# Kernel optimization log

Measured on AMD Instinct MI355X. Metric: run time of the kernel, lower is better.

Reference implementation:

```python
import jax, jax.numpy as jnp
import numpy as np
import math

B, N, D, H, K, W = 2, 2048, 512, 8, 64, 5
HD = D // H      # head_dim = 64
QC = HD // 4     # per-head quaternion component = 16
QI = D // 4      # full-model quaternion component = 128


def _qlinear(x, r, i, j, k, b):
    # Hamilton-product weight matrix, as built in QLinear.forward
    Wm = jnp.concatenate([
        jnp.concatenate([r, -i, -j, -k], 1),
        jnp.concatenate([i,  r, -k,  j], 1),
        jnp.concatenate([j,  k,  r, -i], 1),
        jnp.concatenate([k, -j,  i,  r], 1)], 0)
    return x @ Wm.T + b


def _layernorm(x, g, b, eps=1e-5):
    m = x.mean(-1, keepdims=True)
    v = ((x - m) ** 2).mean(-1, keepdims=True)
    return (x - m) / jnp.sqrt(v + eps) * g + b


def _forward(query, key, value, cross_context, density_feat, mask, time_idx,
             q_r, q_i, q_j, q_k, q_b, k_r, k_i, k_j, k_k, k_b,
             v_w, v_b, o_w, o_b, thr, dm1_w, dm1_b, dm2_w, dm2_b,
             ef, ec, ev_w, ev_b, ln_g, ln_b):
    spike_slope = 5.0
    # ---- QuaternionSpikeAttention (cross_ctx=True, dropout inactive in eval) ----
    q = _qlinear(query, q_r, q_i, q_j, q_k, q_b)
    k = _qlinear(key, k_r, k_i, k_j, k_k, k_b) + _qlinear(cross_context, k_r, k_i, k_j, k_k, k_b)
    v = jnp.concatenate([value, cross_context], -1) @ v_w.T + v_b
    qh = q.reshape(B, N, H, HD)
    kh = k.reshape(B, N, H, HD)
    vh = v.reshape(B, N, H, HD)
    # sum of the 4 quaternion-component dot products == full dot over head_dim
    scores = jnp.einsum('bmhd,bnhd->bhmn', qh, kh) / math.sqrt(QC)
    scores = jnp.clip(scores, -6.0, 6.0)
    base_thr = jax.nn.softplus(thr)
    hdm = jax.nn.gelu(density_feat @ dm1_w.T + dm1_b, approximate=False)
    d_shift = (hdm @ dm2_w.T + dm2_b)[..., 0]                # [B, N]
    threshold = base_thr + d_shift[:, None, None, :] * 0.1   # varies over key index
    gate = jax.nn.sigmoid(spike_slope * (scores - threshold))
    mod = scores * (1.0 + 2.0 * gate)
    m2 = mask[:, None, :, None] * mask[:, None, None, :]     # [B,1,M,N] outer mask
    mod = jnp.where(m2 == 0, -10000.0, mod)
    wts = jax.nn.softmax(jnp.clip(mod, -30.0, 30.0), axis=-1)
    attn = jnp.einsum('bhmn,bnhd->bmhd', wts, vh).reshape(B, N, D)
    attn = attn @ o_w.T + o_b
    # ---- TemporalEventConvolution ----
    order = jnp.argsort(time_idx, axis=1)
    qs = jnp.take_along_axis(query, order[..., None], axis=1)
    ms = jnp.take_along_axis(mask, order, axis=1)
    half = W // 2
    qp = jnp.pad(qs, ((0, 0), (half, half), (0, 0)))
    qwin = jnp.stack([qp[:, w:w + N] for w in range(W)], axis=2)  # [B,N,W,D]
    # quaternion-split filter matching collapses to a full dot over D
    act = jnp.einsum('bnwd,kwd->bnk', qwin, ef) / math.sqrt(QI)
    act = jnp.where(ms[..., None] == 0, -10000.0, act)
    act = jax.nn.softmax(act, axis=-1)
    ctx = act @ ec                                            # [B,N,D]
    ctx = _layernorm(ctx @ ev_w.T + ev_b, ln_g, ln_b) * ms[..., None]
    inv = jnp.argsort(order, axis=1)
    ctx = jnp.take_along_axis(ctx, inv[..., None], axis=1) * mask[..., None]
    return attn + ctx


def setup_inputs() -> dict:
    key0 = jax.random.key(0)
    ks = jax.random.split(key0, 24)
    lim = math.sqrt(6.0 / (QI + QI))
    def xav(k):
        return jax.random.uniform(k, (QI, QI), jnp.float32, -lim, lim)
    def lin(k, o, i):
        l = math.sqrt(1.0 / i)
        return jax.random.uniform(k, (o, i), jnp.float32, -l, l)
    return {
        'query': jax.random.normal(ks[0], (B, N, D), jnp.float32),
        'key': jax.random.normal(ks[1], (B, N, D), jnp.float32),
        'value': jax.random.normal(ks[2], (B, N, D), jnp.float32),
        'cross_context': jax.random.normal(ks[3], (B, N, D), jnp.float32),
        'density_feat': jax.random.normal(ks[4], (B, N, 3), jnp.float32),
        'mask': jnp.ones((B, N), jnp.float32),
        'time_idx': jax.random.randint(ks[5], (B, N), 0, 1000000),
        'q_r': xav(ks[6]), 'q_i': xav(ks[7]), 'q_j': xav(ks[8]), 'q_k': xav(ks[9]),
        'q_b': jnp.zeros((D,), jnp.float32),
        'k_r': xav(ks[10]), 'k_i': xav(ks[11]), 'k_j': xav(ks[12]), 'k_k': xav(ks[13]),
        'k_b': jnp.zeros((D,), jnp.float32),
        'v_w': lin(ks[14], D, 2 * D), 'v_b': jnp.zeros((D,), jnp.float32),
        'o_w': lin(ks[15], D, D), 'o_b': jnp.zeros((D,), jnp.float32),
        'thr': jnp.float32(-1.0),
        'dm1_w': lin(ks[16], 16, 3), 'dm1_b': jnp.zeros((16,), jnp.float32),
        'dm2_w': jnp.zeros((1, 16), jnp.float32), 'dm2_b': jnp.zeros((1,), jnp.float32),
        'ef': jax.random.normal(ks[17], (K, W, D), jnp.float32) * 0.02,
        'ec': jax.random.normal(ks[18], (K, D), jnp.float32) * 0.02,
        'ev_w': lin(ks[19], D, D), 'ev_b': jnp.zeros((D,), jnp.float32),
        'ln_g': jnp.ones((D,), jnp.float32), 'ln_b': jnp.zeros((D,), jnp.float32),
    }


def reference(query, key, value, cross_context, density_feat, mask, time_idx,
              q_r, q_i, q_j, q_k, q_b, k_r, k_i, k_j, k_k, k_b,
              v_w, v_b, o_w, o_b, thr, dm1_w, dm1_b, dm2_w, dm2_b,
              ef, ec, ev_w, ev_b, ln_g, ln_b):
    return _forward(query, key, value, cross_context, density_feat, mask, time_idx,
                    q_r, q_i, q_j, q_k, q_b, k_r, k_i, k_j, k_k, k_b,
                    v_w, v_b, o_w, o_b, thr, dm1_w, dm1_b, dm2_w, dm2_b,
                    ef, ec, ev_w, ev_b, ln_g, ln_b)
```

## Files before the change

kernel.cpp:

```cpp
#include <hip/hip_runtime.h>
#include <math.h>

#define BB 2
#define NN 2048
#define DDIM 512
#define HH 8
#define HDIM 64
#define BN 4096

#define WS_WMQ   0
#define WS_WMK   262144
#define WS_THRK  524288
#define WS_ORDER 528384
#define WS_DKW   532480
#define WS_W5    1843200
#define WS_Q     2105344
#define WS_K     4202496
#define WS_V     6299648
#define PLANE_US 2097152

typedef short bf16x8 __attribute__((ext_vector_type(8)));
typedef float f32x4  __attribute__((ext_vector_type(4)));

__device__ __forceinline__ float4 ld4(const float* p) { return *(const float4*)p; }

__device__ __forceinline__ float red16_max(float v) {
  v = fmaxf(v, __shfl_xor(v, 1, 64));
  v = fmaxf(v, __shfl_xor(v, 2, 64));
  v = fmaxf(v, __shfl_xor(v, 4, 64));
  v = fmaxf(v, __shfl_xor(v, 8, 64));
  return v;
}
__device__ __forceinline__ float red16_sum(float v) {
  v += __shfl_xor(v, 1, 64);
  v += __shfl_xor(v, 2, 64);
  v += __shfl_xor(v, 4, 64);
  v += __shfl_xor(v, 8, 64);
  return v;
}

__device__ __forceinline__ unsigned short f2bu(float f) {
  unsigned u = __float_as_uint(f);
  unsigned r = 0x7FFFu + ((u >> 16) & 1u);
  return (unsigned short)((u + r) >> 16);
}
__device__ __forceinline__ float bu2f(unsigned short u) {
  return __uint_as_float(((unsigned)u) << 16);
}
__device__ __forceinline__ void split2(float x, unsigned short& hi, unsigned short& lo) {
  hi = f2bu(x);
  lo = f2bu(x - bu2f(hi));
}

__global__ __launch_bounds__(256) void build_wm_kernel(
    const float* __restrict__ qr, const float* __restrict__ qi,
    const float* __restrict__ qj, const float* __restrict__ qk,
    const float* __restrict__ kr, const float* __restrict__ ki,
    const float* __restrict__ kj, const float* __restrict__ kk,
    unsigned short* __restrict__ wmqH, unsigned short* __restrict__ wmqL,
    unsigned short* __restrict__ wmkH, unsigned short* __restrict__ wmkL)
{
  int idx = blockIdx.x * 256 + threadIdx.x;
  int sel = idx >> 18;
  int r   = idx & 262143;
  int p = r >> 9, q = r & 511;
  int pb = p >> 7, qb = q >> 7, pr = p & 127, qc = q & 127;
  const int   comp_t[4][4] = {{0,1,2,3},{1,0,3,2},{2,3,0,1},{3,2,1,0}};
  const float sign_t[4][4] = {{1.f,-1.f,-1.f,-1.f},{1.f,1.f,-1.f,1.f},
                              {1.f,1.f,1.f,-1.f},{1.f,-1.f,1.f,1.f}};
  const float* cq[4] = {qr,qi,qj,qk};
  const float* ck[4] = {kr,ki,kj,kk};
  int c = comp_t[pb][qb];
  float s = sign_t[pb][qb];
  const float* src = sel ? ck[c] : cq[c];
  float v = s * src[pr*128 + qc];
  unsigned short hi, lo;
  split2(v, hi, lo);
  if (sel) { wmkH[r] = hi; wmkL[r] = lo; }
  else     { wmqH[r] = hi; wmqL[r] = lo; }
}

__global__ __launch_bounds__(256) void presplit_kernel(
    const float* __restrict__ src, int n4,
    unsigned short* __restrict__ hp, unsigned short* __restrict__ lp)
{
  int i = blockIdx.x * 256 + threadIdx.x;
  if (i >= n4) return;
  float4 v = ((const float4*)src)[i];
  ushort4 h, l;
  split2(v.x, h.x, l.x);  split2(v.y, h.y, l.y);
  split2(v.z, h.z, l.z);  split2(v.w, h.w, l.w);
  ((ushort4*)hp)[i] = h;
  ((ushort4*)lp)[i] = l;
}

__global__ __launch_bounds__(256) void rank_kernel(const int* __restrict__ tidx,
                                                   int* __restrict__ order)
{
  __shared__ int ts[NN];
  int b = blockIdx.y;
  for (int i = threadIdx.x; i < NN; i += 256) ts[i] = tidx[b*NN + i];
  __syncthreads();
  int i = blockIdx.x * 256 + threadIdx.x;
  int ti = ts[i];
  int rank = 0;
  #pragma unroll 4
  for (int j = 0; j < NN; j++) {
    int tj = ts[j];
    rank += (tj < ti || (tj == ti && j < i)) ? 1 : 0;
  }
  order[b*NN + rank] = i;
}

__global__ __launch_bounds__(256) void thr_kernel(
    const float* __restrict__ df, const float* __restrict__ dm1w,
    const float* __restrict__ dm1b, const float* __restrict__ dm2w,
    const float* __restrict__ dm2b, const float* __restrict__ thrp,
    int dm1b_bstride, float* __restrict__ thrK)
{
  int i = blockIdx.x * 256 + threadIdx.x;
  if (i >= BN) return;
  int b = i >> 11;
  const float* bb = dm1b + b*dm1b_bstride;
  float x0 = df[i*3+0], x1 = df[i*3+1], x2 = df[i*3+2];
  float acc = dm2b[0];
  #pragma unroll
  for (int j = 0; j < 16; j++) {
    float h = dm1w[j*3+0]*x0 + dm1w[j*3+1]*x1 + dm1w[j*3+2]*x2 + bb[j];
    h = 0.5f * h * (1.f + erff(h * 0.70710678118654752f));
    acc += h * dm2w[j];
  }
  float tv = thrp[0];
  float base = fmaxf(tv, 0.f) + log1pf(expf(-fabsf(tv)));
  thrK[i] = base + 0.1f * acc;
}

#define GSTR 72
template<int MODE, int OUT, int AP, int BP>
__global__ __launch_bounds__(256) void mgemm_kernel(
    const float* __restrict__ A0, const float* __restrict__ A1,
    const unsigned short* __restrict__ APh, const unsigned short* __restrict__ APl,
    const float* __restrict__ W,
    const unsigned short* __restrict__ BPh, const unsigned short* __restrict__ BPl,
    const float* __restrict__ bias,
    float bias_scale, float scale, float* __restrict__ out,
    int Ka, int N, int ldout)
{
  __shared__ __align__(16) unsigned short AHi[64*GSTR], ALo[64*GSTR];
  __shared__ __align__(16) unsigned short BHi[64*GSTR], BLo[64*GSTR];
  const int t = threadIdx.x;
  const int w = t >> 6, lane = t & 63;
  const int quad = lane >> 4, lm = lane & 15;
  const int m0 = blockIdx.x * 64, n0 = blockIdx.y * 64;
  const int lrr = t >> 4, ld = (t & 15) * 4;

  f32x4 acc[4];
  #pragma unroll
  for (int s = 0; s < 4; s++) acc[s] = (f32x4){0.f,0.f,0.f,0.f};

  for (int k0 = 0; k0 < Ka; k0 += 64) {
    __syncthreads();
    if (AP) {
      #pragma unroll
      for (int i = 0; i < 2; i++) {
        int c = t*2 + i;
        int row = c >> 3, c8 = (c & 7) * 8;
        int off = (m0 + row)*Ka + k0 + c8;
        *(uint4*)&AHi[row*GSTR + c8] = *(const uint4*)&APh[off];
        *(uint4*)&ALo[row*GSTR + c8] = *(const uint4*)&APl[off];
      }
    } else {
      #pragma unroll
      for (int p = 0; p < 4; p++) {
        int row = lrr + p*16;
        float4 av;
        if (MODE == 0) {
          av = ld4(&A0[(size_t)(m0+row)*Ka + k0 + ld]);
        } else if (MODE == 1) {
          float4 x = ld4(&A0[(m0+row)*512 + k0 + ld]);
          float4 y = ld4(&A1[(m0+row)*512 + k0 + ld]);
          av = make_float4(x.x+y.x, x.y+y.y, x.z+y.z, x.w+y.w);
        } else {
          int kg = k0 + ld;
          av = (kg < 512) ? ld4(&A0[(m0+row)*512 + kg])
                          : ld4(&A1[(m0+row)*512 + kg - 512]);
        }
        ushort4 hi, lo;
        split2(av.x, hi.x, lo.x);  split2(av.y, hi.y, lo.y);
        split2(av.z, hi.z, lo.z);  split2(av.w, hi.w, lo.w);
        *(ushort4*)&AHi[row*GSTR + ld] = hi;
        *(ushort4*)&ALo[row*GSTR + ld] = lo;
      }
    }
    if (BP) {
      #pragma unroll
      for (int i = 0; i < 2; i++) {
        int c = t*2 + i;
        int row = c >> 3, c8 = (c & 7) * 8;
        int brow = n0 + row;  if (brow > N-1) brow = N-1;
        int off = brow*Ka + k0 + c8;
        *(uint4*)&BHi[row*GSTR + c8] = *(const uint4*)&BPh[off];
        *(uint4*)&BLo[row*GSTR + c8] = *(const uint4*)&BPl[off];
      }
    } else {
      #pragma unroll
      for (int p = 0; p < 4; p++) {
        int row = lrr + p*16;
        int brow = n0 + row;  if (brow > N-1) brow = N-1;
        float4 wv = ld4(&W[(size_t)brow*Ka + k0 + ld]);
        ushort4 hi, lo;
        split2(wv.x, hi.x, lo.x);  split2(wv.y, hi.y, lo.y);
        split2(wv.z, hi.z, lo.z);  split2(wv.w, hi.w, lo.w);
        *(ushort4*)&BHi[row*GSTR + ld] = hi;
        *(ushort4*)&BLo[row*GSTR + ld] = lo;
      }
    }
    __syncthreads();
    #pragma unroll
    for (int ks = 0; ks < 2; ks++) {
      int arow = (w*16 + lm)*GSTR + ks*32 + quad*8;
      bf16x8 ah = *(const bf16x8*)&AHi[arow];
      bf16x8 al = *(const bf16x8*)&ALo[arow];
      #pragma unroll
      for (int sub = 0; sub < 4; sub++) {
        int baddr = (sub*16 + lm)*GSTR + ks*32 + quad*8;
        bf16x8 bh = *(const bf16x8*)&BHi[baddr];
        bf16x8 bl = *(const bf16x8*)&BLo[baddr];
        acc[sub] = __builtin_amdgcn_mfma_f32_16x16x32_bf16(ah, bh, acc[sub], 0, 0, 0);
        acc[sub] = __builtin_amdgcn_mfma_f32_16x16x32_bf16(ah, bl, acc[sub], 0, 0, 0);
        acc[sub] = __builtin_amdgcn_mfma_f32_16x16x32_bf16(al, bh, acc[sub], 0, 0, 0);
      }
    }
  }
  #pragma unroll
  for (int sub = 0; sub < 4; sub++) {
    int col = n0 + sub*16 + lm;
    if (col >= N) continue;
    float bv = bias ? bias[col] * bias_scale : 0.f;
    if (OUT == 0) {
      #pragma unroll
      for (int r = 0; r < 4; r++) {
        int row = m0 + w*16 + quad*4 + r;
        out[(size_t)row*ldout + col] = acc[sub][r]*scale + bv;
      }
    } else if (OUT == 1) {
      unsigned short* hp = (unsigned short*)out;
      unsigned short* lp = hp + (size_t)4096*ldout;
      #pragma unroll
      for (int r = 0; r < 4; r++) {
        int row = m0 + w*16 + quad*4 + r;
        unsigned short hv, lv;
        split2(acc[sub][r]*scale + bv, hv, lv);
        hp[(size_t)row*ldout + col] = hv;
        lp[(size_t)row*ldout + col] = lv;
      }
    } else {
      unsigned short* hp = (unsigned short*)out;
      unsigned short* lp = hp + (size_t)PLANE_US;
      int hcol = col >> 6, d = col & 63;
      int row0 = m0 + w*16 + quad*4;
      int bb2 = row0 >> 11, n = row0 & 2047;
      unsigned short h0,h1,h2,h3,l0,l1,l2,l3;
      split2(acc[sub][0]*scale + bv, h0, l0);
      split2(acc[sub][1]*scale + bv, h1, l1);
      split2(acc[sub][2]*scale + bv, h2, l2);
      split2(acc[sub][3]*scale + bv, h3, l3);
      size_t vidx = (((size_t)bb2*8 + hcol)*64 + d)*2048 + n;
      *(ushort4*)&hp[vidx] = make_ushort4(h0,h1,h2,h3);
      *(ushort4*)&lp[vidx] = make_ushort4(l0,l1,l2,l3);
    }
  }
}

__global__ __launch_bounds__(256) void t1a_kernel(const float* __restrict__ dkw,
    const int* __restrict__ order, int K, int W, float* __restrict__ w5raw)
{
  int idx = blockIdx.x * 256 + threadIdx.x;
  if (idx >= BN*K) return;
  int k  = idx % K;
  int bn = idx / K;
  int b = bn >> 11, r = bn & 2047;
  const int* ob = order + b*NN;
  int KW = K*W, half = W >> 1;
  float acc = 0.f;
  for (int w = 0; w < W; w++) {
    int rr = r + w - half;
    if (rr < 0 || rr >= NN) continue;
    acc += dkw[(size_t)(b*NN + ob[rr])*KW + k*W + w];
  }
  w5raw[(size_t)(b*NN + ob[r])*K + k] = acc;
}

__global__ __launch_bounds__(256) void t1b_kernel(const float* __restrict__ mask,
    int K, float* __restrict__ w5)
{
  int i = blockIdx.x * 256 + threadIdx.x;
  if (i >= BN) return;
  float* row = w5 + (size_t)i*K;
  if (mask[i] == 0.f) {
    float u = 1.f / (float)K;
    for (int k = 0; k < K; k++) row[k] = u;
    return;
  }
  float mx = -1e30f;
  for (int k = 0; k < K; k++) mx = fmaxf(mx, row[k]);
  float ss = 0.f;
  for (int k = 0; k < K; k++) { float e = __expf(row[k]-mx); row[k] = e; ss += e; }
  float inv = 1.f/ss;
  for (int k = 0; k < K; k++) row[k] *= inv;
}

__global__ __launch_bounds__(256) void ecv_kernel(const float* __restrict__ ec,
    const float* __restrict__ evw, int K, float* __restrict__ ecv)
{
  int idx = blockIdx.x * 256 + threadIdx.x;
  if (idx >= K*512) return;
  int k = idx >> 9, j = idx & 511;
  const float4* e4 = (const float4*)(ec + k*512);
  const float4* w4 = (const float4*)(evw + j*512);
  float acc = 0.f;
  for (int d = 0; d < 128; d++) {
    float4 a = e4[d], b = w4[d];
    acc += a.x*b.x + a.y*b.y + a.z*b.z + a.w*b.w;
  }
  ecv[k*512 + j] = acc;
}

__global__ __launch_bounds__(256) void t2p_kernel(const float* __restrict__ w5,
    const float* __restrict__ ecv, const float* __restrict__ evb,
    int K, float* __restrict__ ctx2)
{
  int idx = blockIdx.x * 256 + threadIdx.x;
  int bn = idx >> 7;
  int q4 = idx & 127;
  const float* wp = w5 + (size_t)bn*K;
  const float4* e4 = (const float4*)ecv;
  float4 bv = ((const float4*)evb)[q4];
  float4 acc = bv;
  for (int k = 0; k < K; k++) {
    float w = wp[k];
    float4 e = e4[k*128 + q4];
    acc.x += w*e.x; acc.y += w*e.y; acc.z += w*e.z; acc.w += w*e.w;
  }
  ((float4*)ctx2)[idx] = acc;
}

#define QSTR 72
__global__ __launch_bounds__(256) void attn_kernel(
    const unsigned short* __restrict__ QHi, const unsigned short* __restrict__ QLo,
    const unsigned short* __restrict__ KHp, const unsigned short* __restrict__ KLp,
    const unsigned short* __restrict__ VtHi, const unsigned short* __restrict__ VtLo,
    const float* __restrict__ thrK, const float* __restrict__ mask,
    unsigned short* __restrict__ AoutH, unsigned short* __restrict__ AoutL)
{
  __shared__ __align__(16) unsigned short KHs[64*QSTR];
  __shared__ __align__(16) unsigned short KLs[64*QSTR];
  __shared__ __align__(16) unsigned short VHs[64*QSTR];
  __shared__ __align__(16) unsigned short VLs[64*QSTR];
  __shared__ float thr_s[64], mk_s[64], mm_s[64];

  const int t = threadIdx.x;
  const int w = t >> 6, lane = t & 63;
  const int quad = lane >> 4, lm = lane & 15;
  const int m0 = blockIdx.x * 64;
  const int bh = blockIdx.y;
  const int b = bh >> 3, h = bh & 7;
  const int base = b*NN*DDIM + h*HDIM;
  const int sr = t >> 3;
  const int sc = (t & 7) * 8;

  bf16x8 qh[2], ql[2];
  {
    size_t qoff = (size_t)(b*NN + m0 + w*16 + lm)*DDIM + h*HDIM + quad*8;
    qh[0] = *(const bf16x8*)&QHi[qoff];
    qh[1] = *(const bf16x8*)&QHi[qoff + 32];
    ql[0] = *(const bf16x8*)&QLo[qoff];
    ql[1] = *(const bf16x8*)&QLo[qoff + 32];
  }
  if (t < 64) mm_s[t] = mask[b*NN + m0 + t];

  f32x4 o_acc[4];
  #pragma unroll
  for (int s = 0; s < 4; s++) o_acc[s] = (f32x4){0.f,0.f,0.f,0.f};
  float m_i[4] = {-1e30f,-1e30f,-1e30f,-1e30f};
  float l_i[4] = {0.f,0.f,0.f,0.f};

  for (int n0 = 0; n0 < NN; n0 += 64) {
    __syncthreads();
    #pragma unroll
    for (int p = 0; p < 2; p++) {
      int row = sr + p*32;
      size_t g  = (size_t)(b*NN + n0 + row)*DDIM + h*HDIM + sc;
      *(uint4*)&KHs[row*QSTR + sc] = *(const uint4*)&KHp[g];
      *(uint4*)&KLs[row*QSTR + sc] = *(const uint4*)&KLp[g];
      size_t gv = ((size_t)bh*HDIM + row)*NN + n0 + sc;
      *(uint4*)&VHs[row*QSTR + sc] = *(const uint4*)&VtHi[gv];
      *(uint4*)&VLs[row*QSTR + sc] = *(const uint4*)&VtLo[gv];
    }
    if (t < 64) { thr_s[t] = thrK[b*NN + n0 + t]; mk_s[t] = mask[b*NN + n0 + t]; }
    __syncthreads();

    f32x4 s_acc[4];
    #pragma unroll
    for (int s = 0; s < 4; s++) s_acc[s] = (f32x4){0.f,0.f,0.f,0.f};
    #pragma unroll
    for (int ks = 0; ks < 2; ks++) {
      #pragma unroll
      for (int sub = 0; sub < 4; sub++) {
        int baddr = (sub*16 + lm)*QSTR + ks*32 + quad*8;
        bf16x8 bh8 = *(const bf16x8*)&KHs[baddr];
        bf16x8 bl8 = *(const bf16x8*)&KLs[baddr];
        s_acc[sub] = __builtin_amdgcn_mfma_f32_16x16x32_bf16(qh[ks], bh8, s_acc[sub], 0, 0, 0);
        s_acc[sub] = __builtin_amdgcn_mfma_f32_16x16x32_bf16(qh[ks], bl8, s_acc[sub], 0, 0, 0);
        s_acc[sub] = __builtin_amdgcn_mfma_f32_16x16x32_bf16(ql[ks], bh8, s_acc[sub], 0, 0, 0);
      }
    }
    __syncthreads();

    float thc5[4], mkc[4];
    #pragma unroll
    for (int sub = 0; sub < 4; sub++) {
      thc5[sub] = 5.f * thr_s[sub*16 + lm];
      mkc[sub] = mk_s[sub*16 + lm];
    }
    float p_[4][4];
    #pragma unroll
    for (int r = 0; r < 4; r++) {
      float mm = mm_s[w*16 + quad*4 + r];
      float rmax = -1e30f;
      float modv[4];
      #pragma unroll
      for (int sub = 0; sub < 4; sub++) {
        float sc2 = s_acc[sub][r]*0.25f;
        sc2 = fminf(fmaxf(sc2,-6.f),6.f);
        float e = __expf(__builtin_fmaf(-5.f, sc2, thc5[sub]));
        float gte = __builtin_amdgcn_rcpf(1.f + e);
        float mv = sc2*(1.f + 2.f*gte);
        if (mm*mkc[sub] == 0.f) mv = -1e4f;
        mv = fminf(fmaxf(mv,-30.f),30.f);
        modv[sub] = mv;
        rmax = fmaxf(rmax, mv);
      }
      rmax = red16_max(rmax);
      float mnew = fmaxf(m_i[r], rmax);
      float scale = __expf(m_i[r]-mnew);
      m_i[r] = mnew;
      float rs = 0.f;
      #pragma unroll
      for (int sub = 0; sub < 4; sub++) { float e = __expf(modv[sub]-mnew); p_[r][sub] = e; rs += e; }
      rs = red16_sum(rs);
      l_i[r] = l_i[r]*scale + rs;
      #pragma unroll
      for (int sub = 0; sub < 4; sub++) o_acc[sub][r] *= scale;
    }
    #pragma unroll
    for (int r = 0; r < 4; r++) {
      int prow = (w*16 + quad*4 + r)*QSTR + lm;
      #pragma unroll
      for (int sub = 0; sub < 4; sub++) {
        unsigned short hi, lo;
        split2(p_[r][sub], hi, lo);
        KHs[prow + sub*16] = hi;
        KLs[prow + sub*16] = lo;
      }
    }
    __syncthreads();

    bf16x8 ph[2], pl[2];
    {
      int arow = (w*16 + lm)*QSTR + quad*8;
      ph[0] = *(const bf16x8*)&KHs[arow];
      ph[1] = *(const bf16x8*)&KHs[arow + 32];
      pl[0] = *(const bf16x8*)&KLs[arow];
      pl[1] = *(const bf16x8*)&KLs[arow + 32];
    }
    #pragma unroll
    for (int ks = 0; ks < 2; ks++) {
      #pragma unroll
      for (int sub = 0; sub < 4; sub++) {
        int baddr = (sub*16 + lm)*QSTR + ks*32 + quad*8;
        bf16x8 vh8 = *(const bf16x8*)&VHs[baddr];
        bf16x8 vl8 = *(const bf16x8*)&VLs[baddr];
        o_acc[sub] = __builtin_amdgcn_mfma_f32_16x16x32_bf16(ph[ks], vh8, o_acc[sub], 0, 0, 0);
        o_acc[sub] = __builtin_amdgcn_mfma_f32_16x16x32_bf16(ph[ks], vl8, o_acc[sub], 0, 0, 0);
        o_acc[sub] = __builtin_amdgcn_mfma_f32_16x16x32_bf16(pl[ks], vh8, o_acc[sub], 0, 0, 0);
      }
    }
  }
  float inv[4];
  #pragma unroll
  for (int r = 0; r < 4; r++) inv[r] = 1.f / l_i[r];
  #pragma unroll
  for (int sub = 0; sub < 4; sub++) {
    #pragma unroll
    for (int r = 0; r < 4; r++) {
      int row = m0 + w*16 + quad*4 + r;
      float val = o_acc[sub][r] * inv[r];
      unsigned short hv, lv;
      split2(val, hv, lv);
      size_t o = (size_t)base + (size_t)row*DDIM + sub*16 + lm;
      AoutH[o] = hv;
      AoutL[o] = lv;
    }
  }
}

__global__ __launch_bounds__(256) void t3_kernel(const float* __restrict__ ctx2,
    const float* __restrict__ lng, const float* __restrict__ lnb,
    const float* __restrict__ mask, const float* __restrict__ outf,
    float* __restrict__ out)
{
  int wid = threadIdx.x >> 6, lane = threadIdx.x & 63;
  int row = blockIdx.x * 4 + wid;
  const float4* x4 = (const float4*)(ctx2 + row*DDIM);
  float4 v0 = x4[lane], v1 = x4[lane+64];
  float s = v0.x+v0.y+v0.z+v0.w + v1.x+v1.y+v1.z+v1.w;
  #pragma unroll
  for (int m = 1; m < 64; m <<= 1) s += __shfl_xor(s, m, 64);
  float mean = s * (1.f/512.f);
  float d0 = v0.x-mean, d1 = v0.y-mean, d2 = v0.z-mean, d3 = v0.w-mean;
  float d4 = v1.x-mean, d5 = v1.y-mean, d6 = v1.z-mean, d7 = v1.w-mean;
  float sq = d0*d0+d1*d1+d2*d2+d3*d3+d4*d4+d5*d5+d6*d6+d7*d7;
  #pragma unroll
  for (int m = 1; m < 64; m <<= 1) sq += __shfl_xor(sq, m, 64);
  float rstd = rsqrtf(sq * (1.f/512.f) + 1e-5f);
  float mk = mask[row];
  float f = mk*mk;
  const float4* g4 = (const float4*)lng;
  const float4* b4 = (const float4*)lnb;
  float4 G0 = g4[lane], G1 = g4[lane+64], B0 = b4[lane], B1 = b4[lane+64];
  float4 O0 = *(const float4*)&outf[row*DDIM + lane*4];
  float4 O1 = *(const float4*)&outf[row*DDIM + (lane+64)*4];
  float4 R0, R1;
  R0.x = O0.x + (d0*rstd*G0.x + B0.x)*f;
  R0.y = O0.y + (d1*rstd*G0.y + B0.y)*f;
  R0.z = O0.z + (d2*rstd*G0.z + B0.z)*f;
  R0.w = O0.w + (d3*rstd*G0.w + B0.w)*f;
  R1.x = O1.x + (d4*rstd*G1.x + B1.x)*f;
  R1.y = O1.y + (d5*rstd*G1.y + B1.y)*f;
  R1.z = O1.z + (d6*rstd*G1.z + B1.z)*f;
  R1.w = O1.w + (d7*rstd*G1.w + B1.w)*f;
  *(float4*)&out[row*DDIM + lane*4] = R0;
  *(float4*)&out[row*DDIM + (lane+64)*4] = R1;
}

__global__ void telem_write_kernel(float val, float* __restrict__ out)
{
  if (threadIdx.x == 0 && blockIdx.x == 0) out[0] = val;
}

extern "C" void kernel_launch(void* const* d_in, const int* in_sizes, int n_in,
                              void* d_out, int out_size, void* d_ws, size_t ws_size,
                              hipStream_t stream)
{
  (void)n_in; (void)out_size; (void)ws_size;
  const float* query = (const float*)d_in[0];
  const float* key_  = (const float*)d_in[1];
  const float* value = (const float*)d_in[2];
  const float* cross = (const float*)d_in[3];
  const float* df    = (const float*)d_in[4];
  const float* mask  = (const float*)d_in[5];
  const int*   tidx  = (const int*)  d_in[6];
  const float* q_r = (const float*)d_in[7],  *q_i = (const float*)d_in[8];
  const float* q_j = (const float*)d_in[9],  *q_k = (const float*)d_in[10];
  const float* q_b = (const float*)d_in[11];
  const float* k_r = (const float*)d_in[12], *k_i = (const float*)d_in[13];
  const float* k_j = (const float*)d_in[14], *k_k = (const float*)d_in[15];
  const float* k_b = (const float*)d_in[16];
  const float* v_w = (const float*)d_in[17], *v_b = (const float*)d_in[18];
  const float* o_w = (const float*)d_in[19], *o_b = (const float*)d_in[20];
  const float* thrp = (const float*)d_in[21];
  const float* dm1w = (const float*)d_in[22], *dm1b = (const float*)d_in[23];
  const float* dm2w = (const float*)d_in[24], *dm2b = (const float*)d_in[25];
  const float* ef   = (const float*)d_in[26], *ec   = (const float*)d_in[27];
  const float* ev_w = (const float*)d_in[28], *ev_b = (const float*)d_in[29];
  const float* lng  = (const float*)d_in[30], *lnb  = (const float*)d_in[31];

  const int s23 = in_sizes[23];
  const int s26 = in_sizes[26];
  const int s27 = in_sizes[27];
  int Kf = (s27 > 0 && s27 % 512 == 0) ? s27 / 512 : 0;
  int Wf = (Kf > 0 && s26 % (Kf*512) == 0) ? s26 / (Kf*512) : 0;
  bool cfg_ok = (Kf >= 1 && Kf <= 64) && (Wf == 1 || Wf == 3 || Wf == 5)
                && (Kf*Wf <= 320);
  if (!cfg_ok) { Kf = 5; Wf = 5; }
  const int KW = Kf * Wf;
  const int dm1b_bstride = (s23 == 32) ? 16 : 0;

  float* ws   = (float*)d_ws;
  float* thrK = ws + WS_THRK;
  int*   order = (int*)(ws + WS_ORDER);
  float* dkw  = ws + WS_DKW;
  float* w5   = ws + WS_W5;
  float* Qb   = ws + WS_Q;
  float* Kb   = ws + WS_K;
  float* Vb   = ws + WS_V;
  float* out  = (float*)d_out;
  float* OutF = Kb;
  float* ctx2 = Qb;

  unsigned short* wmqH = (unsigned short*)(ws + WS_WMQ);
  unsigned short* wmqL = wmqH + 262144;
  unsigned short* wmkH = (unsigned short*)(ws + WS_WMK);
  unsigned short* wmkL = wmkH + 262144;
  unsigned short* qryH = (unsigned short*)d_out;
  unsigned short* qryL = qryH + PLANE_US;
  unsigned short* vwH  = (unsigned short*)(ws + WS_DKW);
  unsigned short* vwL  = vwH + 524288;
  unsigned short* owH  = (unsigned short*)(ws + WS_W5);
  unsigned short* owL  = owH + 262144;
  unsigned short* efH  = (unsigned short*)(ws + WS_WMQ);
  unsigned short* efL  = efH + KW*512;
  float* ecv = ws + WS_WMQ;

  const unsigned short* QHi = (const unsigned short*)Qb;
  const unsigned short* QLo = QHi + PLANE_US;
  const unsigned short* KHp = (const unsigned short*)Kb;
  const unsigned short* KLp = KHp + PLANE_US;
  const unsigned short* VtH = (const unsigned short*)Vb;
  const unsigned short* VtL = VtH + PLANE_US;

  build_wm_kernel<<<2048, 256, 0, stream>>>(q_r,q_i,q_j,q_k, k_r,k_i,k_j,k_k,
                                            wmqH, wmqL, wmkH, wmkL);
  rank_kernel<<<dim3(8,2), 256, 0, stream>>>(tidx, order);
  thr_kernel<<<16, 256, 0, stream>>>(df, dm1w, dm1b, dm2w, dm2b, thrp,
                                     dm1b_bstride, thrK);
  presplit_kernel<<<2048, 256, 0, stream>>>(query, 524288, qryH, qryL);
  presplit_kernel<<<512, 256, 0, stream>>>(v_w, 131072, vwH, vwL);
  presplit_kernel<<<256, 256, 0, stream>>>(o_w, 65536, owH, owL);

  const float rs128 = 0.08838834764831845f;
  mgemm_kernel<0,1,1,1><<<dim3(64,8), 256, 0, stream>>>(
      nullptr, nullptr, qryH, qryL, nullptr, wmqH, wmqL, q_b, 1.f, 1.f, Qb, 512, 512, 512);
  mgemm_kernel<1,1,0,1><<<dim3(64,8), 256, 0, stream>>>(
      key_, cross, nullptr, nullptr, nullptr, wmkH, wmkL, k_b, 2.f, 1.f, Kb, 512, 512, 512);
  presplit_kernel<<<(KW*128 + 255)/256, 256, 0, stream>>>(ef, KW*128, efH, efL);
  mgemm_kernel<2,2,0,1><<<dim3(64,8), 256, 0, stream>>>(
      value, cross, nullptr, nullptr, nullptr, vwH, vwL, v_b, 1.f, 1.f, Vb, 1024, 512, 512);
  mgemm_kernel<0,0,1,1><<<dim3(64,(KW+63)/64), 256, 0, stream>>>(
      nullptr, nullptr, qryH, qryL, nullptr, efH, efL, nullptr, 0.f, rs128, dkw, 512, KW, KW);

  attn_kernel<<<dim3(32,16), 256, 0, stream>>>(QHi, QLo, KHp, KLp, VtH, VtL,
                                               thrK, mask, qryH, qryL);
  mgemm_kernel<0,0,1,1><<<dim3(64,8), 256, 0, stream>>>(
      nullptr, nullptr, qryH, qryL, nullptr, owH, owL, o_b, 1.f, 1.f, OutF, 512, 512, 512);

  t1a_kernel<<<(BN*Kf + 255)/256, 256, 0, stream>>>(dkw, order, Kf, Wf, w5);
  t1b_kernel<<<16, 256, 0, stream>>>(mask, Kf, w5);
  ecv_kernel<<<(Kf*512 + 255)/256, 256, 0, stream>>>(ec, ev_w, Kf, ecv);
  t2p_kernel<<<2048, 256, 0, stream>>>(w5, ecv, ev_b, Kf, ctx2);
  t3_kernel<<<1024, 256, 0, stream>>>(ctx2, lng, lnb, mask, OutF, out);

  if (!cfg_ok) {
    int K2 = (s27 / 512 < 127) ? s27 / 512 : 127;
    telem_write_kernel<<<1, 64, 0, stream>>>(-65536.f * (float)(K2+1), out);
  }
}
```

Measured before the change: 582.1 us.

## Drop online softmax via fixed max bound; split attention block into key halves

The attention kernel drops the running-max online softmax. Since the modulated scores are clamped to [-30,30], it uses a fixed offset of 30, so there are no per-tile max reductions and no rescaling of the accumulators. The row sums are combined across waves only at the end. Each block now handles 32 query rows, with wave pairs splitting the 64-key tile in halves, and the grid doubles. The P-tile stores to LDS now use an XOR swizzle to reduce bank conflicts. The fixed offset risks underflow of exp(mv-30) for rows whose scores are all low (e.g. masked rows at -30), and each block reloads the same K/V tiles for fewer queries, which doubles K/V traffic.

New measurement: 546.1 us. 6.2% less time.

```diff
diff --git a/kernel.cpp b/kernel.cpp
--- a/kernel.cpp
+++ b/kernel.cpp
@@ -24,13 +24,6 @@
 
 __device__ __forceinline__ float4 ld4(const float* p) { return *(const float4*)p; }
 
-__device__ __forceinline__ float red16_max(float v) {
-  v = fmaxf(v, __shfl_xor(v, 1, 64));
-  v = fmaxf(v, __shfl_xor(v, 2, 64));
-  v = fmaxf(v, __shfl_xor(v, 4, 64));
-  v = fmaxf(v, __shfl_xor(v, 8, 64));
-  return v;
-}
 __device__ __forceinline__ float red16_sum(float v) {
   v += __shfl_xor(v, 1, 64);
   v += __shfl_xor(v, 2, 64);
@@ -357,12 +350,14 @@
   __shared__ __align__(16) unsigned short KLs[64*QSTR];
   __shared__ __align__(16) unsigned short VHs[64*QSTR];
   __shared__ __align__(16) unsigned short VLs[64*QSTR];
-  __shared__ float thr_s[64], mk_s[64], mm_s[64];
+  __shared__ float thr_s[64], mk_s[64], mm_s[32];
+  __shared__ float ls[2][32];
 
   const int t = threadIdx.x;
-  const int w = t >> 6, lane = t & 63;
+  const int wv = t >> 6, lane = t & 63;
+  const int g = wv & 1, sh = wv >> 1;
   const int quad = lane >> 4, lm = lane & 15;
-  const int m0 = blockIdx.x * 64;
+  const int m0 = blockIdx.x * 32;
   const int bh = blockIdx.y;
   const int b = bh >> 3, h = bh & 7;
   const int base = b*NN*DDIM + h*HDIM;
@@ -371,28 +366,27 @@
 
   bf16x8 qh[2], ql[2];
   {
-    size_t qoff = (size_t)(b*NN + m0 + w*16 + lm)*DDIM + h*HDIM + quad*8;
+    size_t qoff = (size_t)(b*NN + m0 + g*16 + lm)*DDIM + h*HDIM + quad*8;
     qh[0] = *(const bf16x8*)&QHi[qoff];
     qh[1] = *(const bf16x8*)&QHi[qoff + 32];
     ql[0] = *(const bf16x8*)&QLo[qoff];
     ql[1] = *(const bf16x8*)&QLo[qoff + 32];
   }
-  if (t < 64) mm_s[t] = mask[b*NN + m0 + t];
-
-  f32x4 o_acc[4];
-  #pragma unroll
-  for (int s = 0; s < 4; s++) o_acc[s] = (f32x4){0.f,0.f,0.f,0.f};
-  float m_i[4] = {-1e30f,-1e30f,-1e30f,-1e30f};
-  float l_i[4] = {0.f,0.f,0.f,0.f};
+  if (t < 32) mm_s[t] = mask[b*NN + m0 + t];
+
+  f32x4 o_acc[2];
+  o_acc[0] = (f32x4){0.f,0.f,0.f,0.f};
+  o_acc[1] = (f32x4){0.f,0.f,0.f,0.f};
+  float lsum[4] = {0.f,0.f,0.f,0.f};
 
   for (int n0 = 0; n0 < NN; n0 += 64) {
     __syncthreads();
     #pragma unroll
     for (int p = 0; p < 2; p++) {
       int row = sr + p*32;
-      size_t g  = (size_t)(b*NN + n0 + row)*DDIM + h*HDIM + sc;
-      *(uint4*)&KHs[row*QSTR + sc] = *(const uint4*)&KHp[g];
-      *(uint4*)&KLs[row*QSTR + sc] = *(const uint4*)&KLp[g];
+      size_t gg = (size_t)(b*NN + n0 + row)*DDIM + h*HDIM + sc;
+      *(uint4*)&KHs[row*QSTR + sc] = *(const uint4*)&KHp[gg];
+      *(uint4*)&KLs[row*QSTR + sc] = *(const uint4*)&KLp[gg];
       size_t gv = ((size_t)bh*HDIM + row)*NN + n0 + sc;
       *(uint4*)&VHs[row*QSTR + sc] = *(const uint4*)&VtHi[gv];
       *(uint4*)&VLs[row*QSTR + sc] = *(const uint4*)&VtLo[gv];
@@ -400,105 +394,112 @@
     if (t < 64) { thr_s[t] = thrK[b*NN + n0 + t]; mk_s[t] = mask[b*NN + n0 + t]; }
     __syncthreads();
 
-    f32x4 s_acc[4];
-    #pragma unroll
-    for (int s = 0; s < 4; s++) s_acc[s] = (f32x4){0.f,0.f,0.f,0.f};
+    f32x4 s_acc[2];
+    s_acc[0] = (f32x4){0.f,0.f,0.f,0.f};
+    s_acc[1] = (f32x4){0.f,0.f,0.f,0.f};
     #pragma unroll
     for (int ks = 0; ks < 2; ks++) {
       #pragma unroll
-      for (int sub = 0; sub < 4; sub++) {
+      for (int sl = 0; sl < 2; sl++) {
+        int sub = sh*2 + sl;
         int baddr = (sub*16 + lm)*QSTR + ks*32 + quad*8;
         bf16x8 bh8 = *(const bf16x8*)&KHs[baddr];
         bf16x8 bl8 = *(const bf16x8*)&KLs[baddr];
-        s_acc[sub] = __builtin_amdgcn_mfma_f32_16x16x32_bf16(qh[ks], bh8, s_acc[sub], 0, 0, 0);
-        s_acc[sub] = __builtin_amdgcn_mfma_f32_16x16x32_bf16(qh[ks], bl8, s_acc[sub], 0, 0, 0);
-        s_acc[sub] = __builtin_amdgcn_mfma_f32_16x16x32_bf16(ql[ks], bh8, s_acc[sub], 0, 0, 0);
+        s_acc[sl] = __builtin_amdgcn_mfma_f32_16x16x32_bf16(qh[ks], bh8, s_acc[sl], 0, 0, 0);
+        s_acc[sl] = __builtin_amdgcn_mfma_f32_16x16x32_bf16(qh[ks], bl8, s_acc[sl], 0, 0, 0);
+        s_acc[sl] = __builtin_amdgcn_mfma_f32_16x16x32_bf16(ql[ks], bh8, s_acc[sl], 0, 0, 0);
       }
     }
     __syncthreads();
 
-    float thc5[4], mkc[4];
-    #pragma unroll
-    for (int sub = 0; sub < 4; sub++) {
-      thc5[sub] = 5.f * thr_s[sub*16 + lm];
-      mkc[sub] = mk_s[sub*16 + lm];
-    }
-    float p_[4][4];
+    float thc5[2], mkc[2];
+    #pragma unroll
+    for (int sl = 0; sl < 2; sl++) {
+      int key = (sh*2 + sl)*16 + lm;
+      thc5[sl] = 5.f * thr_s[key];
+      mkc[sl] = mk_s[key];
+    }
+    float p_[4][2];
     #pragma unroll
     for (int r = 0; r < 4; r++) {
-      float mm = mm_s[w*16 + quad*4 + r];
-      float rmax = -1e30f;
-      float modv[4];
-      #pragma unroll
-      for (int sub = 0; sub < 4; sub++) {
-        float sc2 = s_acc[sub][r]*0.25f;
+      float mm = mm_s[g*16 + quad*4 + r];
+      #pragma unroll
+      for (int sl = 0; sl < 2; sl++) {
+        float sc2 = s_acc[sl][r]*0.25f;
         sc2 = fminf(fmaxf(sc2,-6.f),6.f);
-        float e = __expf(__builtin_fmaf(-5.f, sc2, thc5[sub]));
+        float e = __expf(__builtin_fmaf(-5.f, sc2, thc5[sl]));
         float gte = __builtin_amdgcn_rcpf(1.f + e);
         float mv = sc2*(1.f + 2.f*gte);
-        if (mm*mkc[sub] == 0.f) mv = -1e4f;
+        if (mm*mkc[sl] == 0.f) mv = -1e4f;
         mv = fminf(fmaxf(mv,-30.f),30.f);
-        modv[sub] = mv;
-        rmax = fmaxf(rmax, mv);
-      }
-      rmax = red16_max(rmax);
-      float mnew = fmaxf(m_i[r], rmax);
-      float scale = __expf(m_i[r]-mnew);
-      m_i[r] = mnew;
-      float rs = 0.f;
-      #pragma unroll
-      for (int sub = 0; sub < 4; sub++) { float e = __expf(modv[sub]-mnew); p_[r][sub] = e; rs += e; }
-      rs = red16_sum(rs);
-      l_i[r] = l_i[r]*scale + rs;
-      #pragma unroll
-      for (int sub = 0; sub < 4; sub++) o_acc[sub][r] *= scale;
+        float p = __expf(mv - 30.f);
+        p_[r][sl] = p;
+        lsum[r] += p;
+      }
     }
     #pragma unroll
     for (int r = 0; r < 4; r++) {
-      int prow = (w*16 + quad*4 + r)*QSTR + lm;
-      #pragma unroll
-      for (int sub = 0; sub < 4; sub++) {
+      int prow = (g*16 + quad*4 + r)*QSTR;
+      int xk = quad << 3;
+      #pragma unroll
+      for (int sl = 0; sl < 2; sl++) {
+        int cx = (lm + (sh*2+sl)*16) ^ xk;
         unsigned short hi, lo;
-        split2(p_[r][sub], hi, lo);
-        KHs[prow + sub*16] = hi;
-        KLs[prow + sub*16] = lo;
+        split2(p_[r][sl], hi, lo);
+        KHs[prow + cx] = hi;
+        KLs[prow + cx] = lo;
       }
     }
     __syncthreads();
 
     bf16x8 ph[2], pl[2];
     {
-      int arow = (w*16 + lm)*QSTR + quad*8;
-      ph[0] = *(const bf16x8*)&KHs[arow];
-      ph[1] = *(const bf16x8*)&KHs[arow + 32];
-      pl[0] = *(const bf16x8*)&KLs[arow];
-      pl[1] = *(const bf16x8*)&KLs[arow + 32];
+      int arow = (g*16 + lm)*QSTR;
+      int rk = ((lm >> 2) & 3) << 3;
+      int c0 = (quad*8) ^ rk;
+      int c1 = (quad*8 + 32) ^ rk;
+      ph[0] = *(const bf16x8*)&KHs[arow + c0];
+      ph[1] = *(const bf16x8*)&KHs[arow + c1];
+      pl[0] = *(const bf16x8*)&KLs[arow + c0];
+      pl[1] = *(const bf16x8*)&KLs[arow + c1];
     }
     #pragma unroll
     for (int ks = 0; ks < 2; ks++) {
       #pragma unroll
-      for (int sub = 0; sub < 4; sub++) {
+      for (int sl = 0; sl < 2; sl++) {
+        int sub = sh*2 + sl;
         int baddr = (sub*16 + lm)*QSTR + ks*32 + quad*8;
         bf16x8 vh8 = *(const bf16x8*)&VHs[baddr];
         bf16x8 vl8 = *(const bf16x8*)&VLs[baddr];
-        o_acc[sub] = __builtin_amdgcn_mfma_f32_16x16x32_bf16(ph[ks], vh8, o_acc[sub], 0, 0, 0);
-        o_acc[sub] = __builtin_amdgcn_mfma_f32_16x16x32_bf16(ph[ks], vl8, o_acc[sub], 0, 0, 0);
-        o_acc[sub] = __builtin_amdgcn_mfma_f32_16x16x32_bf16(pl[ks], vh8, o_acc[sub], 0, 0, 0);
-      }
-    }
-  }
+        o_acc[sl] = __builtin_amdgcn_mfma_f32_16x16x32_bf16(ph[ks], vh8, o_acc[sl], 0, 0, 0);
+        o_acc[sl] = __builtin_amdgcn_mfma_f32_16x16x32_bf16(ph[ks], vl8, o_acc[sl], 0, 0, 0);
+        o_acc[sl] = __builtin_amdgcn_mfma_f32_16x16x32_bf16(pl[ks], vh8, o_acc[sl], 0, 0, 0);
+      }
+    }
+  }
+
+  __syncthreads();
+  #pragma unroll
+  for (int r = 0; r < 4; r++) {
+    float s = red16_sum(lsum[r]);
+    if (lm == 0) ls[sh][g*16 + quad*4 + r] = s;
+  }
+  __syncthreads();
   float inv[4];
   #pragma unroll
-  for (int r = 0; r < 4; r++) inv[r] = 1.f / l_i[r];
-  #pragma unroll
-  for (int sub = 0; sub < 4; sub++) {
+  for (int r = 0; r < 4; r++) {
+    int rl = g*16 + quad*4 + r;
+    inv[r] = 1.f / (ls[0][rl] + ls[1][rl]);
+  }
+  #pragma unroll
+  for (int sl = 0; sl < 2; sl++) {
     #pragma unroll
     for (int r = 0; r < 4; r++) {
-      int row = m0 + w*16 + quad*4 + r;
-      float val = o_acc[sub][r] * inv[r];
+      int row = m0 + g*16 + quad*4 + r;
+      float val = o_acc[sl][r] * inv[r];
       unsigned short hv, lv;
       split2(val, hv, lv);
-      size_t o = (size_t)base + (size_t)row*DDIM + sub*16 + lm;
+      size_t o = (size_t)base + (size_t)row*DDIM + (sh*2+sl)*16 + lm;
       AoutH[o] = hv;
       AoutL[o] = lv;
     }
@@ -640,7 +641,7 @@
   mgemm_kernel<0,0,1,1><<<dim3(64,(KW+63)/64), 256, 0, stream>>>(
       nullptr, nullptr, qryH, qryL, nullptr, efH, efL, nullptr, 0.f, rs128, dkw, 512, KW, KW);
 
-  attn_kernel<<<dim3(32,16), 256, 0, stream>>>(QHi, QLo, KHp, KLp, VtH, VtL,
+  attn_kernel<<<dim3(64,16), 256, 0, stream>>>(QHi, QLo, KHp, KLp, VtH, VtL,
                                                thrK, mask, qryH, qryL);
   mgemm_kernel<0,0,1,1><<<dim3(64,8), 256, 0, stream>>>(
       nullptr, nullptr, qryH, qryL, nullptr, owH, owL, o_b, 1.f, 1.f, OutF, 512, 512, 512);
```
